# Kernel tuning notes

Hardware: AMD Instinct MI355X
Metric: run time of the kernel (lower is better)

## Reference

```python
import jax, jax.numpy as jnp
import numpy as np

B = 256                       # graphs in batch
NS = [4096, 2048, 1024, 512]  # nodes per graph at each stage (pool halves)
F_IN = 3                      # num_feature
D = 64                        # dim_cell
EPB = [32768, 16384, 8192]    # edges per graph at each layer (deg ~8)
NEG = 0.2                     # GATConv leaky_relu negative slope
EPS = 1e-5                    # BatchNorm eps
L = 3                         # layer_cell


def setup_inputs() -> dict:
    key = jax.random.key(0)
    ks = jax.random.split(key, 16)
    inp = {"x": jax.random.normal(ks[0], (B * NS[0], F_IN), jnp.float32)}
    dims = [F_IN, D, D]
    for i in range(L):
        inp[f"W{i}"] = jax.random.normal(ks[1 + i], (dims[i], D), jnp.float32) / np.sqrt(dims[i]).astype(np.float32)
        inp[f"as{i}"] = jax.random.normal(ks[4 + i], (D,), jnp.float32) * 0.1
        inp[f"ad{i}"] = jax.random.normal(ks[7 + i], (D,), jnp.float32) * 0.1
        inp[f"b{i}"] = jnp.zeros((D,), jnp.float32)
        inp[f"e{i}"] = jax.random.randint(ks[10 + i], (2, EPB[i]), 0, NS[i], jnp.int32)
        # cluster assignment: merge node pairs -> every cluster id occupied
        inp[f"c{i}"] = (jnp.arange(NS[i], dtype=jnp.int32) // 2)
    return inp


def _tile_edges(edge, n_per_graph):
    # replicate per-graph edge list across batch with node offsets, then add self-loops
    offs = (jnp.arange(B, dtype=edge.dtype) * n_per_graph)
    e = (edge[:, None, :] + offs[None, :, None]).reshape(2, -1)  # [2, B*E]
    loops = jnp.arange(B * n_per_graph, dtype=edge.dtype)
    return jnp.concatenate([e, jnp.stack([loops, loops])], axis=1)


def _gat(x, W, a_src, a_dst, bias, edge, n_tot):
    # PyG GATConv, heads=1: shared linear, edge-softmax over incoming edges
    h = x @ W                                # [n_tot, D]
    al_s = h @ a_src                         # [n_tot]
    al_d = h @ a_dst
    src, dst = edge[0], edge[1]              # message src j -> target i
    e = jax.nn.leaky_relu(al_s[src] + al_d[dst], NEG)
    m = jax.ops.segment_max(e, dst, num_segments=n_tot)
    ex = jnp.exp(e - m[dst])
    z = jax.ops.segment_sum(ex, dst, num_segments=n_tot)
    alpha = ex / z[dst]                      # softmax per target node
    out = jax.ops.segment_sum(alpha[:, None] * h[src], dst, num_segments=n_tot)
    return out + bias


def reference(x, W0, as0, ad0, b0, W1, as1, ad1, b1, W2, as2, ad2, b2,
              e0, e1, e2, c0, c1, c2):
    Ws, As, Ad, Bs = [W0, W1, W2], [as0, as1, as2], [ad0, ad1, ad2], [b0, b1, b2]
    Es, Cs = [e0, e1, e2], [c0, c1, c2]
    h = x
    for i in range(L):
        n_tot = B * NS[i]
        edge = _tile_edges(Es[i], NS[i])
        h = jax.nn.relu(_gat(h, Ws[i], As[i], Ad[i], Bs[i], edge, n_tot))
        # cluster max_pool: scatter-max nodes into clusters, offset per graph
        c_out = NS[i + 1]
        seg = (Cs[i][None, :] + (jnp.arange(B, dtype=jnp.int32) * c_out)[:, None]).reshape(-1)
        h = jax.ops.segment_max(h, seg, num_segments=B * c_out)
        # BatchNorm1d(affine=False), training-mode batch statistics
        h = (h - h.mean(axis=0)) * jax.lax.rsqrt(h.var(axis=0) + EPS)
    return h.reshape(B, NS[L] * D)
```

## Files before the change

kernel.cpp:

```cpp
#include <hip/hip_runtime.h>
#include <stdint.h>

#define NEG_SLOPE 0.2f
#define BN_EPS 1e-5f

typedef unsigned short u16;
typedef unsigned int   u32;
typedef __attribute__((ext_vector_type(2))) float  v2f;
typedef __attribute__((ext_vector_type(4))) float  f32x4;
typedef __attribute__((ext_vector_type(8))) short  short8;

__device__ __forceinline__ float lrelu(float x){ return fmaxf(x, NEG_SLOPE*x); }
__device__ __forceinline__ float bf2f(u16 u){ return __uint_as_float(((u32)u) << 16); }
__device__ __forceinline__ u16 f2bf(float f){
  u32 u = __float_as_uint(f);
  return (u16)((u + 0x7fffu + ((u >> 16) & 1u)) >> 16);
}

__global__ __launch_bounds__(256) void init_k(int* __restrict__ counts, u16* __restrict__ s0,
                                              u16* __restrict__ s1, u16* __restrict__ s2,
                                              int nc, int n0, int n1, int n2){
  int t = blockIdx.x*256 + threadIdx.x;
  int y = blockIdx.y;
  if (y==0){ if (t<nc) counts[t]=0; }
  else {
    u16* sd = (y==1)?s0:(y==2)?s1:s2;
    int n   = (y==1)?n0:(y==2)?n1:n2;
    if (t<n) sd[t]=0xFFFFu;
  }
}

__global__ __launch_bounds__(256) void hist_all_k(const int* __restrict__ el0, const int* __restrict__ el1,
                                                  const int* __restrict__ el2, int* __restrict__ c0,
                                                  int* __restrict__ c1, int* __restrict__ c2,
                                                  int n0, int n1, int n2){
  int t = blockIdx.x*256 + threadIdx.x;
  int L = blockIdx.y;
  const int* dst = (L==0)?(el0+n0):(L==1)?(el1+n1):(el2+n2);
  int* counts    = (L==0)?c0:(L==1)?c1:c2;
  int n          = (L==0)?n0:(L==1)?n1:n2;
  if (t < n) atomicAdd(&counts[dst[t]], 1);
}

__global__ __launch_bounds__(1024) void scan_all_k(int* __restrict__ c0, int* __restrict__ c1, int* __restrict__ c2,
                         int* __restrict__ ip0, int* __restrict__ ip1, int* __restrict__ ip2,
                         int* __restrict__ cu0, int* __restrict__ cu1, int* __restrict__ cu2,
                         u16* __restrict__ sd0, u16* __restrict__ sd1, u16* __restrict__ sd2,
                         int n0, int n1, int n2){
  int L = blockIdx.x;
  const int* counts = (L==0)?c0:(L==1)?c1:c2;
  int* indptr2      = (L==0)?ip0:(L==1)?ip1:ip2;
  int* cursor       = (L==0)?cu0:(L==1)?cu1:cu2;
  u16* ell_src      = (L==0)?sd0:(L==1)?sd1:sd2;
  int n             = (L==0)?n0:(L==1)?n1:n2;
  __shared__ int part[1024];
  int tid = threadIdx.x;
  int base = tid*4;
  int v0=0,v1=0,v2=0,v3=0;
  if (base+0<n) v0 = (counts[base+0]+4)&~3;
  if (base+1<n) v1 = (counts[base+1]+4)&~3;
  if (base+2<n) v2 = (counts[base+2]+4)&~3;
  if (base+3<n) v3 = (counts[base+3]+4)&~3;
  part[tid] = v0+v1+v2+v3;
  __syncthreads();
  for (int off=1; off<1024; off<<=1){
    int t2 = (tid>=off)?part[tid-off]:0;
    __syncthreads();
    part[tid] += t2;
    __syncthreads();
  }
  int run = (tid>0)?part[tid-1]:0;
  if (base+0<n){ indptr2[base+0]=run; cursor[base+0]=run+1; ell_src[run]=(u16)(base+0); run+=v0; }
  if (base+1<n){ indptr2[base+1]=run; cursor[base+1]=run+1; ell_src[run]=(u16)(base+1); run+=v1; }
  if (base+2<n){ indptr2[base+2]=run; cursor[base+2]=run+1; ell_src[run]=(u16)(base+2); run+=v2; }
  if (base+3<n){ indptr2[base+3]=run; cursor[base+3]=run+1; ell_src[run]=(u16)(base+3); run+=v3; }
  if (tid==0) indptr2[n] = part[1023];
}

__global__ __launch_bounds__(256) void scatter_all_k(const int* __restrict__ el0, const int* __restrict__ el1,
                         const int* __restrict__ el2, int* __restrict__ cu0, int* __restrict__ cu1,
                         int* __restrict__ cu2, u16* __restrict__ sd0, u16* __restrict__ sd1,
                         u16* __restrict__ sd2, int n0, int n1, int n2){
  int t = blockIdx.x*256 + threadIdx.x;
  int L = blockIdx.y;
  const int* el = (L==0)?el0:(L==1)?el1:el2;
  int* cursor   = (L==0)?cu0:(L==1)?cu1:cu2;
  u16* ell_src  = (L==0)?sd0:(L==1)?sd1:sd2;
  int n         = (L==0)?n0:(L==1)?n1:n2;
  if (t < n){
    int dd = el[n + t];
    int p = atomicAdd(&cursor[dd], 1);
    ell_src[p] = (u16)el[t];
  }
}

__global__ __launch_bounds__(1024) void pairsort_k(const int* __restrict__ c0, const int* __restrict__ c1,
                         const int* __restrict__ c2, u16* __restrict__ pm0, u16* __restrict__ pm1,
                         u16* __restrict__ pm2, int np0, int np1, int np2){
  int L = blockIdx.x;
  const int* counts = (L==0)?c0:(L==1)?c1:c2;
  u16* perm = (L==0)?pm0:(L==1)?pm1:pm2;
  int np    = (L==0)?np0:(L==1)?np1:np2;
  __shared__ int hist[64];
  __shared__ int pos[64];
  int t = threadIdx.x;
  if (t < 64) hist[t] = 0;
  __syncthreads();
  for (int p=t; p<np; p+=1024){
    int k = min(max(counts[2*p], counts[2*p+1]), 63);
    atomicAdd(&hist[k], 1);
  }
  __syncthreads();
  if (t == 0){ int run=0; for (int i=0;i<64;i++){ pos[i]=run; run+=hist[i]; } }
  __syncthreads();
  for (int p=t; p<np; p+=1024){
    int k = min(max(counts[2*p], counts[2*p+1]), 63);
    int q = atomicAdd(&pos[k], 1);
    perm[q] = (u16)p;
  }
}

__global__ __launch_bounds__(256) void gemm3_k(const float* __restrict__ x, const float* __restrict__ Wg,
                        const float* __restrict__ asrc, const float* __restrict__ adst,
                        u16* __restrict__ h, float* __restrict__ als, float* __restrict__ ald, int nrows8)
{
  const int l = threadIdx.x & 63;
  const int g = l >> 3;
  const int o = l & 7;
  float W0[8], W1[8], W2[8];
  float vs0=0.f,vs1=0.f,vs2=0.f,vd0=0.f,vd1=0.f,vd2=0.f;
  #pragma unroll
  for (int j=0;j<8;j++){
    W0[j] = Wg[      o*8 + j];
    W1[j] = Wg[ 64 + o*8 + j];
    W2[j] = Wg[128 + o*8 + j];
    float as = asrc[o*8 + j], ad = adst[o*8 + j];
    vs0 = fmaf(W0[j], as, vs0); vs1 = fmaf(W1[j], as, vs1); vs2 = fmaf(W2[j], as, vs2);
    vd0 = fmaf(W0[j], ad, vd0); vd1 = fmaf(W1[j], ad, vd1); vd2 = fmaf(W2[j], ad, vd2);
  }
  #pragma unroll
  for (int off=1; off<8; off<<=1){
    vs0 += __shfl_xor(vs0,off); vs1 += __shfl_xor(vs1,off); vs2 += __shfl_xor(vs2,off);
    vd0 += __shfl_xor(vd0,off); vd1 += __shfl_xor(vd1,off); vd2 += __shfl_xor(vd2,off);
  }
  int wv = blockIdx.x*4 + (int)(threadIdx.x>>6);
  int stride = gridDim.x*4;
  for (int blk = wv; blk < nrows8; blk += stride){
    int r = blk*8 + g;
    float x0 = x[(size_t)r*3+0];
    float x1 = x[(size_t)r*3+1];
    float x2 = x[(size_t)r*3+2];
    u32 pk[4];
    #pragma unroll
    for (int j=0;j<8;j+=2){
      float a0 = fmaf(x0, W0[j],   fmaf(x1, W1[j],   x2*W2[j]));
      float a1 = fmaf(x0, W0[j+1], fmaf(x1, W1[j+1], x2*W2[j+1]));
      pk[j>>1] = (u32)f2bf(a0) | ((u32)f2bf(a1) << 16);
    }
    ((int4*)(h + ((size_t)r << 6)))[o] = make_int4((int)pk[0],(int)pk[1],(int)pk[2],(int)pk[3]);
    if (o == 0){
      als[r] = fmaf(x2, vs2, fmaf(x1, vs1, x0*vs0));
      ald[r] = fmaf(x2, vd2, fmaf(x1, vd1, x0*vd0));
    }
  }
}

__global__ __launch_bounds__(128) void prep_w_k(const float* __restrict__ W, const float* __restrict__ asrc,
                        const float* __restrict__ adst, const float* __restrict__ scratch, float invN,
                        u16* __restrict__ wswz, float* __restrict__ cvec){
  __shared__ float mean_s[64], rstd_s[64], vs_s[64], vd_s[64], cv_s[64], acc[128];
  int t = threadIdx.x;
  float s = 0.f;
  #pragma unroll 8
  for (int b2=0;b2<256;b2++) s += scratch[b2*128 + t];
  acc[t] = s;
  __syncthreads();
  if (t < 64){
    float m = acc[t]*invN;
    float var = acc[64+t]*invN - m*m;
    mean_s[t] = m; rstd_s[t] = rsqrtf(var + BN_EPS);
  }
  __syncthreads();
  if (t < 64){
    float c = 0.f;
    for (int k=0;k<64;k++) c = fmaf(mean_s[k]*rstd_s[k], W[k*64+t], c);
    cv_s[t] = c; cvec[t] = c;
    float vs = 0.f, vd = 0.f;
    for (int col=0; col<64; col++){
      float wv = W[t*64+col];
      vs = fmaf(wv, asrc[col], vs);
      vd = fmaf(wv, adst[col], vd);
    }
    vs_s[t] = rstd_s[t]*vs; vd_s[t] = rstd_s[t]*vd;
  }
  __syncthreads();
  if (t == 0){
    float cs=0.f, cd=0.f;
    for (int col=0; col<64; col++){ cs = fmaf(cv_s[col], asrc[col], cs); cd = fmaf(cv_s[col], adst[col], cd); }
    cvec[64] = cs; cvec[65] = cd;
  }
  if (t < 64){
    #pragma unroll
    for (int f=0; f<8; f++){
      int tt = f >> 1, ch = f & 1;
      #pragma unroll
      for (int j=0; j<8; j++){
        int k   = ch*32 + (t>>4)*8 + j;
        int col = tt*16 + (t&15);
        wswz[(f*64 + t)*8 + j] = f2bf(rstd_s[k] * W[k*64 + col]);
      }
    }
    #pragma unroll
    for (int f=8; f<10; f++){
      int ch = f - 8;
      #pragma unroll
      for (int j=0; j<8; j++){
        int k = ch*32 + (t>>4)*8 + j;
        int colp = t & 15;
        float val = (colp==0)? vs_s[k] : (colp==1)? vd_s[k] : 0.f;
        wswz[(f*64 + t)*8 + j] = f2bf(val);
      }
    }
  }
}

__global__ __launch_bounds__(256) void gemm64_mfma_k(const u16* __restrict__ Pin, const u16* __restrict__ wswz,
                        const float* __restrict__ cvec,
                        u16* __restrict__ h, float* __restrict__ als, float* __restrict__ ald, int nblk16)
{
  const int l = threadIdx.x & 63;
  const int q = l >> 4;
  const int c = l & 15;
  short8 B[10];
  const int4* wsw = (const int4*)wswz;
  #pragma unroll
  for (int f=0; f<10; f++){
    int4 v = wsw[f*64 + l];
    B[f] = *(short8*)&v;
  }
  float cl[4];
  #pragma unroll
  for (int t=0;t<4;t++) cl[t] = cvec[t*16+c];
  const float const_s = cvec[64], const_d = cvec[65];
  int gw = blockIdx.x*4 + (int)(threadIdx.x>>6);
  int stride = gridDim.x*4;
  for (int blk = gw; blk < nblk16; blk += stride){
    size_t rowbase = (size_t)blk*16;
    const int4* arow = (const int4*)(Pin + (rowbase + c)*64);
    int4 a0v = arow[q];
    int4 a1v = arow[4+q];
    short8 A0 = *(short8*)&a0v, A1 = *(short8*)&a1v;
    f32x4 C0={0.f,0.f,0.f,0.f}, C1=C0, C2=C0, C3=C0, C4=C0;
    C0 = __builtin_amdgcn_mfma_f32_16x16x32_bf16(A0, B[0], C0, 0,0,0);
    C0 = __builtin_amdgcn_mfma_f32_16x16x32_bf16(A1, B[1], C0, 0,0,0);
    C1 = __builtin_amdgcn_mfma_f32_16x16x32_bf16(A0, B[2], C1, 0,0,0);
    C1 = __builtin_amdgcn_mfma_f32_16x16x32_bf16(A1, B[3], C1, 0,0,0);
    C2 = __builtin_amdgcn_mfma_f32_16x16x32_bf16(A0, B[4], C2, 0,0,0);
    C2 = __builtin_amdgcn_mfma_f32_16x16x32_bf16(A1, B[5], C2, 0,0,0);
    C3 = __builtin_amdgcn_mfma_f32_16x16x32_bf16(A0, B[6], C3, 0,0,0);
    C3 = __builtin_amdgcn_mfma_f32_16x16x32_bf16(A1, B[7], C3, 0,0,0);
    C4 = __builtin_amdgcn_mfma_f32_16x16x32_bf16(A0, B[8], C4, 0,0,0);
    C4 = __builtin_amdgcn_mfma_f32_16x16x32_bf16(A1, B[9], C4, 0,0,0);
    #pragma unroll
    for (int t=0;t<4;t++){
      f32x4 C = (t==0)?C0:(t==1)?C1:(t==2)?C2:C3;
      #pragma unroll
      for (int reg=0;reg<4;reg++){
        h[(rowbase + q*4 + reg)*64 + t*16 + c] = f2bf(C[reg] - cl[t]);
      }
    }
    if (c == 0){
      #pragma unroll
      for (int reg=0;reg<4;reg++) als[rowbase + q*4 + reg] = C4[reg] - const_s;
    } else if (c == 1){
      #pragma unroll
      for (int reg=0;reg<4;reg++) ald[rowbase + q*4 + reg] = C4[reg] - const_d;
    }
  }
}

__global__ __launch_bounds__(256) void gat_pool_k(const u16* __restrict__ h, const float* __restrict__ bias,
                      const int* __restrict__ indptr2, const int* __restrict__ counts,
                      const u16* __restrict__ perm, const u16* __restrict__ ell_src,
                      const float* __restrict__ als, const float* __restrict__ ald,
                      u16* __restrict__ P, int log2NS, int nwaves)
{
  const int l = threadIdx.x & 63;
  const int g = l >> 3;
  const int o = l & 7;
  const int NB  = gridDim.x;
  const int bid = blockIdx.x;
  const int lb  = (bid & 7) * (NB >> 3) + (bid >> 3);
  const int wv  = lb * 4 + (int)(threadIdx.x >> 6);
  if (wv >= nwaves) return;
  const int wvu = __builtin_amdgcn_readfirstlane(wv);

  const int wbits = log2NS - 3;
  const int b    = wvu >> wbits;
  const int widx = wvu & ((1 << wbits) - 1);
  const int pairslot = widx*4 + (g >> 1);
  const int prow = perm[pairslot];
  const int d = 2*prow + (g & 1);
  const int nmask = (1 << log2NS) - 1;
  const int base = b << log2NS;

  const char* __restrict__ hbase  = (const char*)(h + ((size_t)base << 6));
  const char* __restrict__ albase = (const char*)(als + base);
  const char* __restrict__ elb    = (const char*)ell_src;
  const u32 olane16 = (u32)o << 4;

  const int p0  = indptr2[d];
  const int cnt = counts[d] + 1;
  const float ald_d = ald[base + d];
  const u32 moff = (u32)p0 << 1;

  v2f a01={0.f,0.f}, a23={0.f,0.f}, a45={0.f,0.f}, a67={0.f,0.f};
  float z = 0.f;

  int m0 = *(const u16*)(elb + moff);
  int m1 = *(const u16*)(elb + moff + 2);
  int m2 = *(const u16*)(elb + moff + 4);
  u32 s0 = (u32)(m0 & nmask);
  int4 H0 = *(const int4*)(hbase + ((s0 << 7) + olane16));
  float al0 = *(const float*)(albase + (s0 << 2));
  u32 s1 = (u32)(m1 & nmask);
  int4 H1 = *(const int4*)(hbase + ((s1 << 7) + olane16));
  float al1 = *(const float*)(albase + (s1 << 2));

  #pragma unroll 4
  for (int it = 0; it < cnt; ++it){
    u32 s2 = (u32)(m2 & nmask);
    int4 Hn = *(const int4*)(hbase + ((s2 << 7) + olane16));
    float al2 = *(const float*)(albase + (s2 << 2));
    int m3 = *(const u16*)(elb + (moff + ((u32)(it + 3) << 1)));
    float t = al0 + ald_d;
    float w = (m0 == 0xFFFF) ? 0.f : __expf(fmaxf(t, NEG_SLOPE*t));
    z += w;
    v2f w2 = {w, w};
    a01 += (v2f){ __uint_as_float(((u32)H0.x) << 16), __uint_as_float(((u32)H0.x) & 0xffff0000u) } * w2;
    a23 += (v2f){ __uint_as_float(((u32)H0.y) << 16), __uint_as_float(((u32)H0.y) & 0xffff0000u) } * w2;
    a45 += (v2f){ __uint_as_float(((u32)H0.z) << 16), __uint_as_float(((u32)H0.z) & 0xffff0000u) } * w2;
    a67 += (v2f){ __uint_as_float(((u32)H0.w) << 16), __uint_as_float(((u32)H0.w) & 0xffff0000u) } * w2;
    m0 = m1; m1 = m2; m2 = m3;
    H0 = H1; al0 = al1;
    H1 = Hn; al1 = al2;
  }

  float rz = __builtin_amdgcn_rcpf(z);
  const float* bp = bias + (o << 3);
  float4 bA = *(const float4*)(bp);
  float4 bB = *(const float4*)(bp + 4);
  float q0 = fmaxf(fmaf(a01.x, rz, bA.x), 0.f);
  float q1 = fmaxf(fmaf(a01.y, rz, bA.y), 0.f);
  float q2 = fmaxf(fmaf(a23.x, rz, bA.z), 0.f);
  float q3 = fmaxf(fmaf(a23.y, rz, bA.w), 0.f);
  float q4 = fmaxf(fmaf(a45.x, rz, bB.x), 0.f);
  float q5 = fmaxf(fmaf(a45.y, rz, bB.y), 0.f);
  float q6 = fmaxf(fmaf(a67.x, rz, bB.z), 0.f);
  float q7 = fmaxf(fmaf(a67.y, rz, bB.w), 0.f);
  q0 = fmaxf(q0, __shfl_xor(q0, 8));
  q1 = fmaxf(q1, __shfl_xor(q1, 8));
  q2 = fmaxf(q2, __shfl_xor(q2, 8));
  q3 = fmaxf(q3, __shfl_xor(q3, 8));
  q4 = fmaxf(q4, __shfl_xor(q4, 8));
  q5 = fmaxf(q5, __shfl_xor(q5, 8));
  q6 = fmaxf(q6, __shfl_xor(q6, 8));
  q7 = fmaxf(q7, __shfl_xor(q7, 8));
  if ((g & 1) == 0){
    u32 w0 = (u32)f2bf(q0) | ((u32)f2bf(q1) << 16);
    u32 w1 = (u32)f2bf(q2) | ((u32)f2bf(q3) << 16);
    u32 w2p = (u32)f2bf(q4) | ((u32)f2bf(q5) << 16);
    u32 w3 = (u32)f2bf(q6) | ((u32)f2bf(q7) << 16);
    char* Pb = (char*)P + (((size_t)b << (log2NS - 1)) << 7);
    *(int4*)(Pb + (((u32)prow << 7) + olane16)) = make_int4((int)w0,(int)w1,(int)w2p,(int)w3);
  }
}

__global__ __launch_bounds__(256) void bn_stats_k(const u16* __restrict__ P, float* __restrict__ scratch, int iters){
  const int l = threadIdx.x & 63;
  int gw = blockIdx.x*4 + (threadIdx.x>>6);
  int GW = gridDim.x*4;
  float s = 0.f, s2 = 0.f;
  #pragma unroll 4
  for (int i = 0; i < iters; i++){
    int r = gw + i*GW;
    float v = bf2f(P[(size_t)r*64 + l]);
    s += v; s2 = fmaf(v, v, s2);
  }
  __shared__ float ls[256], ls2[256];
  ls[threadIdx.x] = s; ls2[threadIdx.x] = s2;
  __syncthreads();
  if (threadIdx.x < 64){
    float S  = ls[threadIdx.x] + ls[threadIdx.x+64] + ls[threadIdx.x+128] + ls[threadIdx.x+192];
    float S2 = ls2[threadIdx.x] + ls2[threadIdx.x+64] + ls2[threadIdx.x+128] + ls2[threadIdx.x+192];
    scratch[blockIdx.x*128 + threadIdx.x] = S;
    scratch[blockIdx.x*128 + 64 + threadIdx.x] = S2;
  }
}

__global__ __launch_bounds__(128) void bn_finish_k(const float* __restrict__ scratch, float* __restrict__ stats,
                                                   int nblocks, float invN){
  __shared__ float accs[128];
  int j = threadIdx.x;
  float s = 0.f;
  #pragma unroll 8
  for (int b=0;b<nblocks;b++) s += scratch[b*128 + j];
  accs[j] = s;
  __syncthreads();
  if (j < 64){
    float m = accs[j]*invN;
    float var = accs[j+64]*invN - m*m;
    stats[j] = m;
    stats[64+j] = rsqrtf(var + BN_EPS);
  }
}

__global__ __launch_bounds__(256) void bn_apply_k(const u32* __restrict__ P2, const float* __restrict__ stats,
                                                  float4* __restrict__ out, int nq){
  int t = blockIdx.x*256 + threadIdx.x;
  if (t >= nq) return;
  int l = (t*4) & 63;
  u32 v0 = P2[t*2], v1 = P2[t*2+1];
  float4 r;
  r.x = (__uint_as_float((v0 & 0xffffu) << 16) - stats[l+0]) * stats[64+l+0];
  r.y = (__uint_as_float( v0 & 0xffff0000u    ) - stats[l+1]) * stats[64+l+1];
  r.z = (__uint_as_float((v1 & 0xffffu) << 16) - stats[l+2]) * stats[64+l+2];
  r.w = (__uint_as_float( v1 & 0xffff0000u    ) - stats[l+3]) * stats[64+l+3];
  out[t] = r;
}

extern "C" void kernel_launch(void* const* d_in, const int* in_sizes, int n_in,
                              void* d_out, int out_size, void* d_ws, size_t ws_size,
                              hipStream_t stream)
{
  const float* x      = (const float*)d_in[0];
  const float* Wl[3]  = {(const float*)d_in[1], (const float*)d_in[7],  (const float*)d_in[13]};
  const float* asl[3] = {(const float*)d_in[2], (const float*)d_in[8],  (const float*)d_in[14]};
  const float* adl[3] = {(const float*)d_in[3], (const float*)d_in[9],  (const float*)d_in[15]};
  const float* bl[3]  = {(const float*)d_in[4], (const float*)d_in[10], (const float*)d_in[16]};
  const int*   el[3]  = {(const int*)d_in[5],   (const int*)d_in[11],   (const int*)d_in[17]};

  const int NS[4]  = {4096, 2048, 1024, 512};
  const int EPB[3] = {32768, 16384, 8192};
  const int LOG2NS[3] = {12, 11, 10};
  const int ECAP[3] = {32768+4*4096, 16384+4*2048, 8192+4*1024};
  const int BATCH = 256;

  char* ws = (char*)d_ws;
  size_t off = 0;
  auto alloc = [&](size_t bytes)->char*{
    char* p = ws + off; off += (bytes + 255) & ~(size_t)255; return p;
  };

  u16*   hbuf    = (u16*)alloc((size_t)BATCH*NS[0]*64*2);
  u16*   Pbuf    = (u16*)alloc((size_t)BATCH*NS[1]*64*2);
  float* als     = (float*)alloc((size_t)BATCH*NS[0]*4);
  float* ald     = (float*)alloc((size_t)BATCH*NS[0]*4);
  float* scratch = (float*)alloc(256*128*4);
  float* stats   = (float*)alloc(128*4);
  u16*   wswz    = (u16*)alloc(10*64*8*2);
  float* cvec    = (float*)alloc(128*4);
  int* counts_all = (int*)alloc((size_t)(NS[0]+NS[1]+NS[2])*4);
  int* cursor_all = (int*)alloc((size_t)(NS[0]+NS[1]+NS[2])*4);
  int *counts[3], *cursor[3], *indptr2[3];
  u16* ell_src[3];
  u16* perm[3];
  counts[0]=counts_all; counts[1]=counts_all+NS[0]; counts[2]=counts_all+NS[0]+NS[1];
  cursor[0]=cursor_all; cursor[1]=cursor_all+NS[0]; cursor[2]=cursor_all+NS[0]+NS[1];
  for (int i=0;i<3;i++){
    indptr2[i] = (int*)alloc((size_t)(NS[i]+1)*4);
    ell_src[i] = (u16*)alloc((size_t)(ECAP[i]+16)*2);
    perm[i]    = (u16*)alloc((size_t)NS[i]);
  }
  if (off > ws_size) return;

  int ctot = NS[0]+NS[1]+NS[2];
  {
    dim3 ginit((ECAP[0]+16+255)/256, 4);
    init_k<<<ginit, 256, 0, stream>>>(counts_all, ell_src[0], ell_src[1], ell_src[2],
                                      ctot, ECAP[0]+16, ECAP[1]+16, ECAP[2]+16);
    dim3 ghist(EPB[0]/256, 3);
    hist_all_k<<<ghist, 256, 0, stream>>>(el[0], el[1], el[2], counts[0], counts[1], counts[2],
                                          EPB[0], EPB[1], EPB[2]);
    scan_all_k<<<3, 1024, 0, stream>>>(counts[0], counts[1], counts[2],
                                       indptr2[0], indptr2[1], indptr2[2],
                                       cursor[0], cursor[1], cursor[2],
                                       ell_src[0], ell_src[1], ell_src[2],
                                       NS[0], NS[1], NS[2]);
    scatter_all_k<<<ghist, 256, 0, stream>>>(el[0], el[1], el[2],
                                             cursor[0], cursor[1], cursor[2],
                                             ell_src[0], ell_src[1], ell_src[2],
                                             EPB[0], EPB[1], EPB[2]);
    pairsort_k<<<3, 1024, 0, stream>>>(counts[0], counts[1], counts[2],
                                       perm[0], perm[1], perm[2],
                                       NS[0]/2, NS[1]/2, NS[2]/2);
  }

  for (int i=0;i<3;i++){
    int ntot = BATCH*NS[i];

    if (i==0){
      gemm3_k<<<1024, 256, 0, stream>>>(x, Wl[0], asl[0], adl[0], hbuf, als, ald, ntot/8);
    } else {
      float invN = 1.0f / (float)(BATCH*NS[i]);
      prep_w_k<<<1, 128, 0, stream>>>(Wl[i], asl[i], adl[i], scratch, invN, wswz, cvec);
      gemm64_mfma_k<<<2048, 256, 0, stream>>>(Pbuf, wswz, cvec, hbuf, als, ald, ntot/16);
    }

    int nwaves = ntot/8;
    gat_pool_k<<<nwaves/4, 256, 0, stream>>>(hbuf, bl[i], indptr2[i], counts[i], perm[i],
                                             ell_src[i], als, ald,
                                             Pbuf, LOG2NS[i], nwaves);

    bn_stats_k<<<256, 256, 0, stream>>>(Pbuf, scratch, (ntot/2)/1024);
  }

  bn_finish_k<<<1, 128, 0, stream>>>(scratch, stats, 256, 1.0f/(float)(BATCH*NS[3]));
  int nq = out_size/4;
  bn_apply_k<<<(nq+255)/256, 256, 0, stream>>>((const u32*)Pbuf, stats, (float4*)d_out, nq);
}
```

Measured before the change: 524.1 us.

## Precompute per-edge attention weights in a separate kernel stored as fp16

```diff
diff --git a/kernel.cpp b/kernel.cpp
--- a/kernel.cpp
+++ b/kernel.cpp
@@ -46,12 +46,14 @@
                          int* __restrict__ ip0, int* __restrict__ ip1, int* __restrict__ ip2,
                          int* __restrict__ cu0, int* __restrict__ cu1, int* __restrict__ cu2,
                          u16* __restrict__ sd0, u16* __restrict__ sd1, u16* __restrict__ sd2,
+                         u16* __restrict__ dd0, u16* __restrict__ dd1, u16* __restrict__ dd2,
                          int n0, int n1, int n2){
   int L = blockIdx.x;
   const int* counts = (L==0)?c0:(L==1)?c1:c2;
   int* indptr2      = (L==0)?ip0:(L==1)?ip1:ip2;
   int* cursor       = (L==0)?cu0:(L==1)?cu1:cu2;
   u16* ell_src      = (L==0)?sd0:(L==1)?sd1:sd2;
+  u16* ell_dst      = (L==0)?dd0:(L==1)?dd1:dd2;
   int n             = (L==0)?n0:(L==1)?n1:n2;
   __shared__ int part[1024];
   int tid = threadIdx.x;
@@ -70,27 +72,30 @@
     __syncthreads();
   }
   int run = (tid>0)?part[tid-1]:0;
-  if (base+0<n){ indptr2[base+0]=run; cursor[base+0]=run+1; ell_src[run]=(u16)(base+0); run+=v0; }
-  if (base+1<n){ indptr2[base+1]=run; cursor[base+1]=run+1; ell_src[run]=(u16)(base+1); run+=v1; }
-  if (base+2<n){ indptr2[base+2]=run; cursor[base+2]=run+1; ell_src[run]=(u16)(base+2); run+=v2; }
-  if (base+3<n){ indptr2[base+3]=run; cursor[base+3]=run+1; ell_src[run]=(u16)(base+3); run+=v3; }
+  if (base+0<n){ indptr2[base+0]=run; cursor[base+0]=run+1; ell_src[run]=(u16)(base+0); ell_dst[run]=(u16)(base+0); run+=v0; }
+  if (base+1<n){ indptr2[base+1]=run; cursor[base+1]=run+1; ell_src[run]=(u16)(base+1); ell_dst[run]=(u16)(base+1); run+=v1; }
+  if (base+2<n){ indptr2[base+2]=run; cursor[base+2]=run+1; ell_src[run]=(u16)(base+2); ell_dst[run]=(u16)(base+2); run+=v2; }
+  if (base+3<n){ indptr2[base+3]=run; cursor[base+3]=run+1; ell_src[run]=(u16)(base+3); ell_dst[run]=(u16)(base+3); run+=v3; }
   if (tid==0) indptr2[n] = part[1023];
 }
 
 __global__ __launch_bounds__(256) void scatter_all_k(const int* __restrict__ el0, const int* __restrict__ el1,
                          const int* __restrict__ el2, int* __restrict__ cu0, int* __restrict__ cu1,
                          int* __restrict__ cu2, u16* __restrict__ sd0, u16* __restrict__ sd1,
-                         u16* __restrict__ sd2, int n0, int n1, int n2){
+                         u16* __restrict__ sd2, u16* __restrict__ dd0, u16* __restrict__ dd1,
+                         u16* __restrict__ dd2, int n0, int n1, int n2){
   int t = blockIdx.x*256 + threadIdx.x;
   int L = blockIdx.y;
   const int* el = (L==0)?el0:(L==1)?el1:el2;
   int* cursor   = (L==0)?cu0:(L==1)?cu1:cu2;
   u16* ell_src  = (L==0)?sd0:(L==1)?sd1:sd2;
+  u16* ell_dst  = (L==0)?dd0:(L==1)?dd1:dd2;
   int n         = (L==0)?n0:(L==1)?n1:n2;
   if (t < n){
     int dd = el[n + t];
     int p = atomicAdd(&cursor[dd], 1);
     ell_src[p] = (u16)el[t];
+    ell_dst[p] = (u16)dd;
   }
 }
 
@@ -118,6 +123,23 @@
     int q = atomicAdd(&pos[k], 1);
     perm[q] = (u16)p;
   }
+}
+
+__global__ __launch_bounds__(256) void weight_k(const u16* __restrict__ ell_src,
+                        const u16* __restrict__ ell_dst, const float* __restrict__ als,
+                        const float* __restrict__ ald, _Float16* __restrict__ elw,
+                        int log2NS, int ecap){
+  int slot = blockIdx.x*256 + threadIdx.x;
+  int g = blockIdx.y;
+  if (slot >= ecap) return;
+  int m = ell_src[slot];
+  int nmask = (1 << log2NS) - 1;
+  int s = m & nmask;
+  int d = ell_dst[slot] & nmask;
+  int base = g << log2NS;
+  float a = als[base + s] + ald[base + d];
+  float w = (m == 0xFFFF) ? 0.f : __expf(fmaxf(a, NEG_SLOPE*a));
+  elw[(size_t)g*ecap + slot] = (_Float16)w;
 }
 
 __global__ __launch_bounds__(256) void gemm3_k(const float* __restrict__ x, const float* __restrict__ Wg,
@@ -282,8 +304,8 @@
 __global__ __launch_bounds__(256) void gat_pool_k(const u16* __restrict__ h, const float* __restrict__ bias,
                       const int* __restrict__ indptr2, const int* __restrict__ counts,
                       const u16* __restrict__ perm, const u16* __restrict__ ell_src,
-                      const float* __restrict__ als, const float* __restrict__ ald,
-                      u16* __restrict__ P, int log2NS, int nwaves)
+                      const _Float16* __restrict__ elw,
+                      u16* __restrict__ P, int log2NS, int ecap, int nwaves)
 {
   const int l = threadIdx.x & 63;
   const int g = l >> 3;
@@ -305,45 +327,40 @@
   const int base = b << log2NS;
 
   const char* __restrict__ hbase  = (const char*)(h + ((size_t)base << 6));
-  const char* __restrict__ albase = (const char*)(als + base);
   const char* __restrict__ elb    = (const char*)ell_src;
+  const char* __restrict__ wbase  = (const char*)(elw + (size_t)b * ecap);
   const u32 olane16 = (u32)o << 4;
 
   const int p0  = indptr2[d];
   const int cnt = counts[d] + 1;
-  const float ald_d = ald[base + d];
   const u32 moff = (u32)p0 << 1;
 
   v2f a01={0.f,0.f}, a23={0.f,0.f}, a45={0.f,0.f}, a67={0.f,0.f};
   float z = 0.f;
 
-  int m0 = *(const u16*)(elb + moff);
-  int m1 = *(const u16*)(elb + moff + 2);
+  u32 s0 = (u32)(*(const u16*)(elb + moff)) & nmask;
+  int4 H0 = *(const int4*)(hbase + ((s0 << 7) + olane16));
+  float w0f = (float)*(const _Float16*)(wbase + moff);
+  u32 s1 = (u32)(*(const u16*)(elb + moff + 2)) & nmask;
+  int4 H1 = *(const int4*)(hbase + ((s1 << 7) + olane16));
+  float w1f = (float)*(const _Float16*)(wbase + moff + 2);
   int m2 = *(const u16*)(elb + moff + 4);
-  u32 s0 = (u32)(m0 & nmask);
-  int4 H0 = *(const int4*)(hbase + ((s0 << 7) + olane16));
-  float al0 = *(const float*)(albase + (s0 << 2));
-  u32 s1 = (u32)(m1 & nmask);
-  int4 H1 = *(const int4*)(hbase + ((s1 << 7) + olane16));
-  float al1 = *(const float*)(albase + (s1 << 2));
 
   #pragma unroll 4
   for (int it = 0; it < cnt; ++it){
-    u32 s2 = (u32)(m2 & nmask);
+    u32 s2 = (u32)m2 & nmask;
     int4 Hn = *(const int4*)(hbase + ((s2 << 7) + olane16));
-    float al2 = *(const float*)(albase + (s2 << 2));
+    float w2f = (float)*(const _Float16*)(wbase + (moff + ((u32)(it + 2) << 1)));
     int m3 = *(const u16*)(elb + (moff + ((u32)(it + 3) << 1)));
-    float t = al0 + ald_d;
-    float w = (m0 == 0xFFFF) ? 0.f : __expf(fmaxf(t, NEG_SLOPE*t));
-    z += w;
-    v2f w2 = {w, w};
+    z += w0f;
+    v2f w2 = {w0f, w0f};
     a01 += (v2f){ __uint_as_float(((u32)H0.x) << 16), __uint_as_float(((u32)H0.x) & 0xffff0000u) } * w2;
     a23 += (v2f){ __uint_as_float(((u32)H0.y) << 16), __uint_as_float(((u32)H0.y) & 0xffff0000u) } * w2;
     a45 += (v2f){ __uint_as_float(((u32)H0.z) << 16), __uint_as_float(((u32)H0.z) & 0xffff0000u) } * w2;
     a67 += (v2f){ __uint_as_float(((u32)H0.w) << 16), __uint_as_float(((u32)H0.w) & 0xffff0000u) } * w2;
-    m0 = m1; m1 = m2; m2 = m3;
-    H0 = H1; al0 = al1;
-    H1 = Hn; al1 = al2;
+    m2 = m3;
+    H0 = H1; H1 = Hn;
+    w0f = w1f; w1f = w2f;
   }
 
   float rz = __builtin_amdgcn_rcpf(z);
@@ -456,6 +473,7 @@
   u16*   Pbuf    = (u16*)alloc((size_t)BATCH*NS[1]*64*2);
   float* als     = (float*)alloc((size_t)BATCH*NS[0]*4);
   float* ald     = (float*)alloc((size_t)BATCH*NS[0]*4);
+  u16*   elw     = (u16*)alloc(((size_t)BATCH*ECAP[0] + 16)*2);
   float* scratch = (float*)alloc(256*128*4);
   float* stats   = (float*)alloc(128*4);
   u16*   wswz    = (u16*)alloc(10*64*8*2);
@@ -464,12 +482,14 @@
   int* cursor_all = (int*)alloc((size_t)(NS[0]+NS[1]+NS[2])*4);
   int *counts[3], *cursor[3], *indptr2[3];
   u16* ell_src[3];
+  u16* ell_dst[3];
   u16* perm[3];
   counts[0]=counts_all; counts[1]=counts_all+NS[0]; counts[2]=counts_all+NS[0]+NS[1];
   cursor[0]=cursor_all; cursor[1]=cursor_all+NS[0]; cursor[2]=cursor_all+NS[0]+NS[1];
   for (int i=0;i<3;i++){
     indptr2[i] = (int*)alloc((size_t)(NS[i]+1)*4);
     ell_src[i] = (u16*)alloc((size_t)(ECAP[i]+16)*2);
+    ell_dst[i] = (u16*)alloc((size_t)(ECAP[i]+16)*2);
     perm[i]    = (u16*)alloc((size_t)NS[i]);
   }
   if (off > ws_size) return;
@@ -486,10 +506,12 @@
                                        indptr2[0], indptr2[1], indptr2[2],
                                        cursor[0], cursor[1], cursor[2],
                                        ell_src[0], ell_src[1], ell_src[2],
+                                       ell_dst[0], ell_dst[1], ell_dst[2],
                                        NS[0], NS[1], NS[2]);
     scatter_all_k<<<ghist, 256, 0, stream>>>(el[0], el[1], el[2],
                                              cursor[0], cursor[1], cursor[2],
                                              ell_src[0], ell_src[1], ell_src[2],
+                                             ell_dst[0], ell_dst[1], ell_dst[2],
                                              EPB[0], EPB[1], EPB[2]);
     pairsort_k<<<3, 1024, 0, stream>>>(counts[0], counts[1], counts[2],
                                        perm[0], perm[1], perm[2],
@@ -507,10 +529,13 @@
       gemm64_mfma_k<<<2048, 256, 0, stream>>>(Pbuf, wswz, cvec, hbuf, als, ald, ntot/16);
     }
 
+    weight_k<<<dim3(ECAP[i]/256, BATCH), 256, 0, stream>>>(ell_src[i], ell_dst[i], als, ald,
+                                                           (_Float16*)elw, LOG2NS[i], ECAP[i]);
+
     int nwaves = ntot/8;
     gat_pool_k<<<nwaves/4, 256, 0, stream>>>(hbuf, bl[i], indptr2[i], counts[i], perm[i],
-                                             ell_src[i], als, ald,
-                                             Pbuf, LOG2NS[i], nwaves);
+                                             ell_src[i], (const _Float16*)elw,
+                                             Pbuf, LOG2NS[i], ECAP[i], nwaves);
 
     bn_stats_k<<<256, 256, 0, stream>>>(Pbuf, scratch, (ntot/2)/1024);
   }
```

Result: slower. 572.6 us (+9.2%).
